# Kernel optimization log

Hardware: AMD Instinct MI355X
Metric: run time of the kernel (lower is better)

The kernel has to match this reference:

```python
import jax, jax.numpy as jnp
import numpy as np

N_NODES = 100000
N_EDGES = 800000
D_IN = 128
D_OUT = 128
E_DIM = 16


def setup_inputs() -> dict:
    key = jax.random.key(0)
    k1, k2, k3, k4, k5 = jax.random.split(key, 5)
    x = jax.random.normal(k1, (N_NODES, D_IN), dtype=jnp.float32)
    edge_index = jax.random.randint(k2, (2, N_EDGES), 0, N_NODES, dtype=jnp.int64)
    edge_attr = jax.random.normal(k3, (N_EDGES, E_DIM), dtype=jnp.float32)
    # xavier-uniform-like init scales
    W = jax.random.uniform(k4, (D_IN, D_OUT), dtype=jnp.float32,
                           minval=-1.0, maxval=1.0) * float(np.sqrt(6.0 / (D_IN + D_OUT)))
    edge_w = jax.random.uniform(k5, (E_DIM, D_OUT), dtype=jnp.float32,
                                minval=-1.0, maxval=1.0) * float(np.sqrt(6.0 / (E_DIM + D_OUT)))
    b = jnp.zeros((D_OUT,), dtype=jnp.float32)
    return {"x": x, "edge_index": edge_index, "edge_attr": edge_attr,
            "W": W, "edge_w": edge_w, "b": b}


def reference(x, edge_index, edge_attr, W, edge_w, b):
    src, dst = edge_index[0], edge_index[1]
    xw = x @ W                                   # [N, D_OUT]
    ew = edge_attr @ edge_w                      # [E, D_OUT]
    msg = xw[src] * ew                           # gather + per-edge modulate
    out = jax.ops.segment_sum(msg, dst, num_segments=x.shape[0])  # scatter-add
    out = out + b
    return out
```

## Files before the change

kernel.cpp:

```cpp
#include <hip/hip_runtime.h>
#include <hip/hip_bf16.h>

typedef __bf16 bf16x8 __attribute__((ext_vector_type(8)));
typedef float f32x4 __attribute__((ext_vector_type(4)));

#define D 128
#define EDIM 16
#define CAP 40

__device__ inline unsigned short f2bf(float f) {
    unsigned u = __builtin_bit_cast(unsigned, f);
    u += 0x7fffu + ((u >> 16) & 1u);
    return (unsigned short)(u >> 16);
}

__global__ __launch_bounds__(256) void fill_buckets(
    const int* __restrict__ ei,
    int* __restrict__ deg,
    int2* __restrict__ perm2,
    int E)
{
    const int e = blockIdx.x * 256 + threadIdx.x;
    if (e >= E) return;
    const int src = ei[e];
    const int dst = ei[(size_t)E + e];
    const int pos = atomicAdd(&deg[dst], 1);
    if (pos < CAP) perm2[(size_t)dst * CAP + pos] = make_int2(e, src);
}

__global__ __launch_bounds__(256) void gemm_xw(
    const float* __restrict__ x,
    const float* __restrict__ W,
    unsigned short* __restrict__ xwb,
    int ntiles)
{
    __shared__ unsigned short Wt[128][136];
    const int t = threadIdx.x;

    #pragma unroll
    for (int i = 0; i < 16; ++i) {
        int id = (i * 256 + t) * 4;
        float4 p = *(const float4*)(W + id);
        int k = id >> 7, n = id & 127;
        Wt[n + 0][k] = f2bf(p.x);
        Wt[n + 1][k] = f2bf(p.y);
        Wt[n + 2][k] = f2bf(p.z);
        Wt[n + 3][k] = f2bf(p.w);
    }
    __syncthreads();

    const int wave = t >> 6, lane = t & 63;
    const int quad = lane >> 4, low = lane & 15;
    const int nwaves = gridDim.x * 4;

    for (int mt = blockIdx.x * 4 + wave; mt < ntiles; mt += nwaves) {
        const int arow = mt * 16 + low;
        f32x4 acc[8];
        #pragma unroll
        for (int nt = 0; nt < 8; ++nt) acc[nt] = (f32x4){0.f, 0.f, 0.f, 0.f};

        #pragma unroll
        for (int kc = 0; kc < 4; ++kc) {
            const int k0 = kc * 32 + quad * 8;
            const float* xp = x + (size_t)arow * D + k0;
            float4 a0 = *(const float4*)xp;
            float4 a1 = *(const float4*)(xp + 4);
            union { unsigned short us[8]; bf16x8 v; } a;
            a.us[0] = f2bf(a0.x); a.us[1] = f2bf(a0.y);
            a.us[2] = f2bf(a0.z); a.us[3] = f2bf(a0.w);
            a.us[4] = f2bf(a1.x); a.us[5] = f2bf(a1.y);
            a.us[6] = f2bf(a1.z); a.us[7] = f2bf(a1.w);
            #pragma unroll
            for (int nt = 0; nt < 8; ++nt) {
                bf16x8 bf = *(const bf16x8*)(&Wt[nt * 16 + low][k0]);
                acc[nt] = __builtin_amdgcn_mfma_f32_16x16x32_bf16(a.v, bf, acc[nt], 0, 0, 0);
            }
        }
        #pragma unroll
        for (int nt = 0; nt < 8; ++nt) {
            #pragma unroll
            for (int r = 0; r < 4; ++r) {
                const size_t row = (size_t)mt * 16 + quad * 4 + r;
                xwb[row * D + nt * 16 + low] = f2bf(acc[nt][r]);
            }
        }
    }
}

__global__ __launch_bounds__(256, 6) void gather_out(
    const float* __restrict__ ea,
    const float* __restrict__ ew,
    const unsigned short* __restrict__ xwb,
    const int* __restrict__ deg,
    const int2* __restrict__ perm2,
    const float* __restrict__ b,
    float* __restrict__ out,
    int N)
{
    __shared__ float eas[4][128];
    const int t = threadIdx.x, wave = t >> 6, lane = t & 63;
    const int ch = lane * 2;
    float* const my = eas[wave];

    float c0[16], c1[16];
    #pragma unroll
    for (int k = 0; k < 16; ++k) {
        c0[k] = ew[k * D + ch];
        c1[k] = ew[k * D + ch + 1];
    }
    const float b0 = b[ch], b1 = b[ch + 1];

    const int nw = gridDim.x * 4;
    const int lrow = lane >> 3;
    const int lcol = (lane & 7) * 2;

    for (int n = blockIdx.x * 4 + wave; n < N; n += nw) {
        const int nb = __builtin_amdgcn_readfirstlane(n);
        int dg = deg[nb]; dg = dg < CAP ? dg : CAP;
        const int2* __restrict__ pp = perm2 + (size_t)nb * CAP;
        float a0 = b0, a1 = b1;

        for (int base = 0; base < dg; base += 8) {
            const int rem = dg - base;

            const int ridx = lrow < rem ? lrow : rem - 1;
            const int2 sl = pp[base + ridx];

            const float2 v = *(const float2*)(ea + (size_t)(unsigned)sl.x * EDIM + lcol);
            *(float2*)(my + lane * 2) = v;

            int s[8];
            #pragma unroll
            for (int i = 0; i < 8; ++i)
                s[i] = __builtin_amdgcn_readlane(sl.y, i * 8);

            unsigned xv[8];
            #pragma unroll
            for (int i = 0; i < 8; ++i)
                xv[i] = *(const unsigned*)(xwb + (size_t)(unsigned)s[i] * D + ch);

            asm volatile("" ::: "memory");

            #pragma unroll
            for (int i = 0; i < 8; ++i) {
                const float4* r4 = (const float4*)(my + i * 16);
                const float4 r0 = r4[0], r1 = r4[1], r2 = r4[2], r3 = r4[3];
                float m0 = r0.x * c0[0];
                m0 = fmaf(r0.y, c0[1],  m0); m0 = fmaf(r0.z, c0[2],  m0);
                m0 = fmaf(r0.w, c0[3],  m0); m0 = fmaf(r1.x, c0[4],  m0);
                m0 = fmaf(r1.y, c0[5],  m0); m0 = fmaf(r1.z, c0[6],  m0);
                m0 = fmaf(r1.w, c0[7],  m0); m0 = fmaf(r2.x, c0[8],  m0);
                m0 = fmaf(r2.y, c0[9],  m0); m0 = fmaf(r2.z, c0[10], m0);
                m0 = fmaf(r2.w, c0[11], m0); m0 = fmaf(r3.x, c0[12], m0);
                m0 = fmaf(r3.y, c0[13], m0); m0 = fmaf(r3.z, c0[14], m0);
                m0 = fmaf(r3.w, c0[15], m0);
                float m1 = r0.x * c1[0];
                m1 = fmaf(r0.y, c1[1],  m1); m1 = fmaf(r0.z, c1[2],  m1);
                m1 = fmaf(r0.w, c1[3],  m1); m1 = fmaf(r1.x, c1[4],  m1);
                m1 = fmaf(r1.y, c1[5],  m1); m1 = fmaf(r1.z, c1[6],  m1);
                m1 = fmaf(r1.w, c1[7],  m1); m1 = fmaf(r2.x, c1[8],  m1);
                m1 = fmaf(r2.y, c1[9],  m1); m1 = fmaf(r2.z, c1[10], m1);
                m1 = fmaf(r2.w, c1[11], m1); m1 = fmaf(r3.x, c1[12], m1);
                m1 = fmaf(r3.y, c1[13], m1); m1 = fmaf(r3.z, c1[14], m1);
                m1 = fmaf(r3.w, c1[15], m1);
                const bool act = i < rem;
                const float xlo = act ? __builtin_bit_cast(float, xv[i] << 16) : 0.f;
                const float xhi = act ? __builtin_bit_cast(float, xv[i] & 0xffff0000u) : 0.f;
                a0 = fmaf(m0, xlo, a0);
                a1 = fmaf(m1, xhi, a1);
            }
        }

        *(float2*)(out + (size_t)n * D + ch) = make_float2(a0, a1);
    }
}

extern "C" void kernel_launch(void* const* d_in, const int* in_sizes, int n_in,
                              void* d_out, int out_size, void* d_ws, size_t ws_size,
                              hipStream_t stream) {
    const float* x  = (const float*)d_in[0];
    const int*   ei = (const int*)d_in[1];
    const float* ea = (const float*)d_in[2];
    const float* W  = (const float*)d_in[3];
    const float* ew = (const float*)d_in[4];
    const float* bb = (const float*)d_in[5];
    float* out = (float*)d_out;

    const int N = in_sizes[0] / D;
    const int E = in_sizes[2] / EDIM;

    unsigned short* xwb = (unsigned short*)d_ws;
    int* deg   = (int*)(xwb + (size_t)N * D);
    int2* perm2 = (int2*)(deg + N);

    hipMemsetAsync(deg, 0, (size_t)N * sizeof(int), stream);
    fill_buckets<<<(E + 255) / 256, 256, 0, stream>>>(ei, deg, perm2, E);

    const int ntiles = N / 16;
    gemm_xw<<<(ntiles + 3) / 4, 256, 0, stream>>>(x, W, xwb, ntiles);

    gather_out<<<6144, 256, 0, stream>>>(ea, ew, xwb, deg, perm2, bb, out, N);
}
```

Before: 303.4 us.

## Fuse bucket fill with GEMM and prefetch next node's edge list in gather

The bucket-fill and x@W GEMM kernels are merged into one launch, interleaving blocks (one GEMM block per two fill blocks) so the atomic scatter and the MFMA work can share the GPU at once. The gather kernel now software-pipelines across nodes: it loads the next node's degree and first slot batch while processing the current one. Inactive lanes are masked by zeroing the indices and loads instead of clamping them. The gather's launch-bounds occupancy hint rises from 6 to 8, which adds register pressure. The batch body moves into a macro so the prefetch can sit inside the first batch.

```diff
diff --git a/kernel.cpp b/kernel.cpp
--- a/kernel.cpp
+++ b/kernel.cpp
@@ -14,28 +14,34 @@
     return (unsigned short)(u >> 16);
 }
 
-__global__ __launch_bounds__(256) void fill_buckets(
+__global__ __launch_bounds__(256) void prep_fused(
+    const float* __restrict__ x,
+    const float* __restrict__ W,
+    unsigned short* __restrict__ xwb,
+    int ntiles,
     const int* __restrict__ ei,
     int* __restrict__ deg,
     int2* __restrict__ perm2,
     int E)
 {
-    const int e = blockIdx.x * 256 + threadIdx.x;
-    if (e >= E) return;
-    const int src = ei[e];
-    const int dst = ei[(size_t)E + e];
-    const int pos = atomicAdd(&deg[dst], 1);
-    if (pos < CAP) perm2[(size_t)dst * CAP + pos] = make_int2(e, src);
-}
-
-__global__ __launch_bounds__(256) void gemm_xw(
-    const float* __restrict__ x,
-    const float* __restrict__ W,
-    unsigned short* __restrict__ xwb,
-    int ntiles)
-{
     __shared__ unsigned short Wt[128][136];
     const int t = threadIdx.x;
+    const int bid = blockIdx.x;
+
+    if (bid % 3 != 0) {
+        const int fill_id = bid - bid / 3 - 1;
+        const int e = fill_id * 256 + t;
+        if (e < E) {
+            const int src = ei[e];
+            const int dst = ei[(size_t)E + e];
+            const int pos = atomicAdd(&deg[dst], 1);
+            if (pos < CAP) perm2[(size_t)dst * CAP + pos] = make_int2(e, src);
+        }
+        return;
+    }
+
+    const int gemm_id = bid / 3;
+    const int ngemm = (gridDim.x + 2) / 3;
 
     #pragma unroll
     for (int i = 0; i < 16; ++i) {
@@ -51,9 +57,9 @@
 
     const int wave = t >> 6, lane = t & 63;
     const int quad = lane >> 4, low = lane & 15;
-    const int nwaves = gridDim.x * 4;
-
-    for (int mt = blockIdx.x * 4 + wave; mt < ntiles; mt += nwaves) {
+    const int nwaves = ngemm * 4;
+
+    for (int mt = gemm_id * 4 + wave; mt < ntiles; mt += nwaves) {
         const int arow = mt * 16 + low;
         f32x4 acc[8];
         #pragma unroll
@@ -87,7 +93,60 @@
     }
 }
 
-__global__ __launch_bounds__(256, 6) void gather_out(
+#define BATCH(SL, BASE, DG, PRE)                                              \
+    {                                                                         \
+        const int rem = (DG) - (BASE);                           \
+             \
+        const int erow = (lrow < rem) ? (SL).x : 0;                           \
+        const float2 v = *(const float2*)(ea + (size_t)(unsigned)erow * EDIM + lcol); \
+        *(float2*)(my + lane * 2) = v;                                        \
+                        \
+        int s[8];                                                             \
+        _Pragma("unroll")                                                     \
+        for (int i = 0; i < 8; ++i) {                                         \
+            const int sr = __builtin_amdgcn_readlane((SL).y, i * 8);          \
+            s[i] = (i < rem) ? sr : 0;                                        \
+        }                                                                     \
+                      \
+        unsigned xv[8];                                                       \
+        _Pragma("unroll")                                                     \
+        for (int i = 0; i < 8; ++i) {                                         \
+            const unsigned u = *(const unsigned*)(xwb + (size_t)(unsigned)s[i] * D + ch); \
+            xv[i] = (i < rem) ? u : 0u;                                       \
+        }                                                                     \
+        PRE                                                                   \
+        asm volatile("" ::: "memory");                                        \
+                  \
+        _Pragma("unroll")                                                     \
+        for (int i = 0; i < 8; ++i) {                                         \
+            const float4* r4 = (const float4*)(my + i * 16);                  \
+            const float4 r0 = r4[0], r1 = r4[1], r2 = r4[2], r3 = r4[3];      \
+            float m0 = r0.x * c0[0];                                          \
+            m0 = fmaf(r0.y, c0[1],  m0); m0 = fmaf(r0.z, c0[2],  m0);         \
+            m0 = fmaf(r0.w, c0[3],  m0); m0 = fmaf(r1.x, c0[4],  m0);         \
+            m0 = fmaf(r1.y, c0[5],  m0); m0 = fmaf(r1.z, c0[6],  m0);         \
+            m0 = fmaf(r1.w, c0[7],  m0); m0 = fmaf(r2.x, c0[8],  m0);         \
+            m0 = fmaf(r2.y, c0[9],  m0); m0 = fmaf(r2.z, c0[10], m0);         \
+            m0 = fmaf(r2.w, c0[11], m0); m0 = fmaf(r3.x, c0[12], m0);         \
+            m0 = fmaf(r3.y, c0[13], m0); m0 = fmaf(r3.z, c0[14], m0);         \
+            m0 = fmaf(r3.w, c0[15], m0);                                      \
+            float m1 = r0.x * c1[0];                                          \
+            m1 = fmaf(r0.y, c1[1],  m1); m1 = fmaf(r0.z, c1[2],  m1);         \
+            m1 = fmaf(r0.w, c1[3],  m1); m1 = fmaf(r1.x, c1[4],  m1);         \
+            m1 = fmaf(r1.y, c1[5],  m1); m1 = fmaf(r1.z, c1[6],  m1);         \
+            m1 = fmaf(r1.w, c1[7],  m1); m1 = fmaf(r2.x, c1[8],  m1);         \
+            m1 = fmaf(r2.y, c1[9],  m1); m1 = fmaf(r2.z, c1[10], m1);         \
+            m1 = fmaf(r2.w, c1[11], m1); m1 = fmaf(r3.x, c1[12], m1);         \
+            m1 = fmaf(r3.y, c1[13], m1); m1 = fmaf(r3.z, c1[14], m1);         \
+            m1 = fmaf(r3.w, c1[15], m1);                                      \
+            const float xlo = __builtin_bit_cast(float, xv[i] << 16);         \
+            const float xhi = __builtin_bit_cast(float, xv[i] & 0xffff0000u); \
+            a0 = fmaf(m0, xlo, a0);                                           \
+            a1 = fmaf(m1, xhi, a1);                                           \
+        }                                                                     \
+    }
+
+__global__ __launch_bounds__(256, 8) void gather_out(
     const float* __restrict__ ea,
     const float* __restrict__ ew,
     const unsigned short* __restrict__ xwb,
@@ -114,64 +173,39 @@
     const int lrow = lane >> 3;
     const int lcol = (lane & 7) * 2;
 
-    for (int n = blockIdx.x * 4 + wave; n < N; n += nw) {
-        const int nb = __builtin_amdgcn_readfirstlane(n);
-        int dg = deg[nb]; dg = dg < CAP ? dg : CAP;
-        const int2* __restrict__ pp = perm2 + (size_t)nb * CAP;
+    int n = blockIdx.x * 4 + wave;
+    if (n >= N) return;
+
+    int nb = __builtin_amdgcn_readfirstlane(n);
+    int dg = deg[nb]; dg = dg < CAP ? dg : CAP;
+    int2 slp = perm2[(size_t)nb * CAP + lrow];
+
+    for (;;) {
+        const int nn = n + nw;
         float a0 = b0, a1 = b1;
-
-        for (int base = 0; base < dg; base += 8) {
-            const int rem = dg - base;
-
-            const int ridx = lrow < rem ? lrow : rem - 1;
-            const int2 sl = pp[base + ridx];
-
-            const float2 v = *(const float2*)(ea + (size_t)(unsigned)sl.x * EDIM + lcol);
-            *(float2*)(my + lane * 2) = v;
-
-            int s[8];
-            #pragma unroll
-            for (int i = 0; i < 8; ++i)
-                s[i] = __builtin_amdgcn_readlane(sl.y, i * 8);
-
-            unsigned xv[8];
-            #pragma unroll
-            for (int i = 0; i < 8; ++i)
-                xv[i] = *(const unsigned*)(xwb + (size_t)(unsigned)s[i] * D + ch);
-
-            asm volatile("" ::: "memory");
-
-            #pragma unroll
-            for (int i = 0; i < 8; ++i) {
-                const float4* r4 = (const float4*)(my + i * 16);
-                const float4 r0 = r4[0], r1 = r4[1], r2 = r4[2], r3 = r4[3];
-                float m0 = r0.x * c0[0];
-                m0 = fmaf(r0.y, c0[1],  m0); m0 = fmaf(r0.z, c0[2],  m0);
-                m0 = fmaf(r0.w, c0[3],  m0); m0 = fmaf(r1.x, c0[4],  m0);
-                m0 = fmaf(r1.y, c0[5],  m0); m0 = fmaf(r1.z, c0[6],  m0);
-                m0 = fmaf(r1.w, c0[7],  m0); m0 = fmaf(r2.x, c0[8],  m0);
-                m0 = fmaf(r2.y, c0[9],  m0); m0 = fmaf(r2.z, c0[10], m0);
-                m0 = fmaf(r2.w, c0[11], m0); m0 = fmaf(r3.x, c0[12], m0);
-                m0 = fmaf(r3.y, c0[13], m0); m0 = fmaf(r3.z, c0[14], m0);
-                m0 = fmaf(r3.w, c0[15], m0);
-                float m1 = r0.x * c1[0];
-                m1 = fmaf(r0.y, c1[1],  m1); m1 = fmaf(r0.z, c1[2],  m1);
-                m1 = fmaf(r0.w, c1[3],  m1); m1 = fmaf(r1.x, c1[4],  m1);
-                m1 = fmaf(r1.y, c1[5],  m1); m1 = fmaf(r1.z, c1[6],  m1);
-                m1 = fmaf(r1.w, c1[7],  m1); m1 = fmaf(r2.x, c1[8],  m1);
-                m1 = fmaf(r2.y, c1[9],  m1); m1 = fmaf(r2.z, c1[10], m1);
-                m1 = fmaf(r2.w, c1[11], m1); m1 = fmaf(r3.x, c1[12], m1);
-                m1 = fmaf(r3.y, c1[13], m1); m1 = fmaf(r3.z, c1[14], m1);
-                m1 = fmaf(r3.w, c1[15], m1);
-                const bool act = i < rem;
-                const float xlo = act ? __builtin_bit_cast(float, xv[i] << 16) : 0.f;
-                const float xhi = act ? __builtin_bit_cast(float, xv[i] & 0xffff0000u) : 0.f;
-                a0 = fmaf(m0, xlo, a0);
-                a1 = fmaf(m1, xhi, a1);
+        const int dgc = dg;
+        const size_t ppb = (size_t)nb * CAP;
+
+        int nn_nb = 0, nn_dg = 0;
+        int2 nn_sl = make_int2(0, 0);
+
+        BATCH(slp, 0, dgc,
+            if (nn < N) {
+                nn_nb = __builtin_amdgcn_readfirstlane(nn);
+                nn_dg = deg[nn_nb]; nn_dg = nn_dg < CAP ? nn_dg : CAP;
+                nn_sl = perm2[(size_t)nn_nb * CAP + lrow];
             }
+        )
+
+        for (int base = 8; base < dgc; base += 8) {
+            const int2 sl = perm2[ppb + base + lrow];
+            BATCH(sl, base, dgc, )
         }
 
         *(float2*)(out + (size_t)n * D + ch) = make_float2(a0, a1);
+
+        if (nn >= N) break;
+        n = nn; nb = nn_nb; dg = nn_dg; slp = nn_sl;
     }
 }
 
@@ -194,10 +228,12 @@
     int2* perm2 = (int2*)(deg + N);
 
     hipMemsetAsync(deg, 0, (size_t)N * sizeof(int), stream);
-    fill_buckets<<<(E + 255) / 256, 256, 0, stream>>>(ei, deg, perm2, E);
 
     const int ntiles = N / 16;
-    gemm_xw<<<(ntiles + 3) / 4, 256, 0, stream>>>(x, W, xwb, ntiles);
+    const int nfill  = (E + 255) / 256;
+    const int ngemm  = (ntiles + 3) / 4;
+    prep_fused<<<nfill + ngemm, 256, 0, stream>>>(x, W, xwb, ntiles,
+                                                  ei, deg, perm2, E);
 
     gather_out<<<6144, 256, 0, stream>>>(ea, ew, xwb, deg, perm2, bb, out, N);
 }
```

Result: slower. 373.6 us (+23.1%).

## Fuse bucket fill and XW GEMM into one launch; add nontemporal gather hints

Applied to the files above, without the earlier changes.

The edge-bucketing kernel and the x@W bf16 MFMA GEMM are merged into a single launch. Block IDs are interleaved so two of every three blocks do bucket filling and one does GEMM tiles, letting the atomic-heavy scatter overlap the compute-bound GEMM and removing one kernel launch boundary. Separately, the gather kernel now reads edge_attr with nontemporal loads and writes the output with nontemporal stores, to avoid polluting cache with single-use data. A side cost is that fill blocks still reserve the GEMM's LDS tile, which can limit how many blocks fit per CU.

```diff
diff --git a/kernel.cpp b/kernel.cpp
--- a/kernel.cpp
+++ b/kernel.cpp
@@ -14,28 +14,34 @@
     return (unsigned short)(u >> 16);
 }
 
-__global__ __launch_bounds__(256) void fill_buckets(
+__global__ __launch_bounds__(256) void prep_fused(
+    const float* __restrict__ x,
+    const float* __restrict__ W,
+    unsigned short* __restrict__ xwb,
+    int ntiles,
     const int* __restrict__ ei,
     int* __restrict__ deg,
     int2* __restrict__ perm2,
     int E)
 {
-    const int e = blockIdx.x * 256 + threadIdx.x;
-    if (e >= E) return;
-    const int src = ei[e];
-    const int dst = ei[(size_t)E + e];
-    const int pos = atomicAdd(&deg[dst], 1);
-    if (pos < CAP) perm2[(size_t)dst * CAP + pos] = make_int2(e, src);
-}
-
-__global__ __launch_bounds__(256) void gemm_xw(
-    const float* __restrict__ x,
-    const float* __restrict__ W,
-    unsigned short* __restrict__ xwb,
-    int ntiles)
-{
     __shared__ unsigned short Wt[128][136];
     const int t = threadIdx.x;
+    const int bid = blockIdx.x;
+
+    if (bid % 3 != 0) {
+        const int fill_id = bid - bid / 3 - 1;
+        const int e = fill_id * 256 + t;
+        if (e < E) {
+            const int src = ei[e];
+            const int dst = ei[(size_t)E + e];
+            const int pos = atomicAdd(&deg[dst], 1);
+            if (pos < CAP) perm2[(size_t)dst * CAP + pos] = make_int2(e, src);
+        }
+        return;
+    }
+
+    const int gemm_id = bid / 3;
+    const int ngemm = (gridDim.x + 2) / 3;
 
     #pragma unroll
     for (int i = 0; i < 16; ++i) {
@@ -51,9 +57,9 @@
 
     const int wave = t >> 6, lane = t & 63;
     const int quad = lane >> 4, low = lane & 15;
-    const int nwaves = gridDim.x * 4;
-
-    for (int mt = blockIdx.x * 4 + wave; mt < ntiles; mt += nwaves) {
+    const int nwaves = ngemm * 4;
+
+    for (int mt = gemm_id * 4 + wave; mt < ntiles; mt += nwaves) {
         const int arow = mt * 16 + low;
         f32x4 acc[8];
         #pragma unroll
@@ -126,7 +132,10 @@
             const int ridx = lrow < rem ? lrow : rem - 1;
             const int2 sl = pp[base + ridx];
 
-            const float2 v = *(const float2*)(ea + (size_t)(unsigned)sl.x * EDIM + lcol);
+            const float* ep = ea + (size_t)(unsigned)sl.x * EDIM + lcol;
+            float2 v;
+            v.x = __builtin_nontemporal_load(ep);
+            v.y = __builtin_nontemporal_load(ep + 1);
             *(float2*)(my + lane * 2) = v;
 
             int s[8];
@@ -171,7 +180,9 @@
             }
         }
 
-        *(float2*)(out + (size_t)n * D + ch) = make_float2(a0, a1);
+        float* op = out + (size_t)n * D + ch;
+        __builtin_nontemporal_store(a0, op);
+        __builtin_nontemporal_store(a1, op + 1);
     }
 }
 
@@ -194,10 +205,12 @@
     int2* perm2 = (int2*)(deg + N);
 
     hipMemsetAsync(deg, 0, (size_t)N * sizeof(int), stream);
-    fill_buckets<<<(E + 255) / 256, 256, 0, stream>>>(ei, deg, perm2, E);
 
     const int ntiles = N / 16;
-    gemm_xw<<<(ntiles + 3) / 4, 256, 0, stream>>>(x, W, xwb, ntiles);
+    const int nfill  = (E + 255) / 256;
+    const int ngemm  = (ntiles + 3) / 4;
+    prep_fused<<<nfill + ngemm, 256, 0, stream>>>(x, W, xwb, ntiles,
+                                                  ei, deg, perm2, E);
 
     gather_out<<<6144, 256, 0, stream>>>(ea, ew, xwb, deg, perm2, bb, out, N);
 }
```

After: 287.3 us. 5.3% less time.
